# Kernel optimization log

Hardware: AMD Instinct MI355X
Metric: run time of the kernel (lower is better)

The kernel has to match this reference:

```python
import jax, jax.numpy as jnp
import numpy as np

N = 50000      # nodes
E = 800000     # edges (avg degree 16)
IN = 128       # input feature dim
H = 128        # hidden dim (all layers output H; out_channels unused in source)
DROP_P = 0.5


def setup_inputs() -> dict:
    key = jax.random.key(0)
    ks = jax.random.split(key, 8)
    s_in = 1.0 / np.sqrt(IN).astype(np.float32)
    s_h = 1.0 / np.sqrt(H).astype(np.float32)
    return {
        "x": jax.random.normal(ks[0], (N, IN), jnp.float32),
        "edge_index": jax.random.randint(ks[1], (2, E), 0, N, dtype=jnp.int32),
        "Wl0": jax.random.normal(ks[2], (H, IN), jnp.float32) * s_in,
        "bl0": jnp.zeros((H,), jnp.float32),
        "Wr0": jax.random.normal(ks[3], (H, IN), jnp.float32) * s_in,
        "Wl1": jax.random.normal(ks[4], (H, H), jnp.float32) * s_h,
        "bl1": jnp.zeros((H,), jnp.float32),
        "Wr1": jax.random.normal(ks[5], (H, H), jnp.float32) * s_h,
    }


def _sage_conv(x, src, dst, Wl, bl, Wr):
    # mean-aggregate neighbor messages: gather x[src], scatter-add to dst
    agg = jax.ops.segment_sum(x[src], dst, num_segments=N)          # [N, D]
    deg = jax.ops.segment_sum(jnp.ones((src.shape[0],), x.dtype), dst,
                              num_segments=N)                        # [N]
    agg = agg / jnp.maximum(deg, 1.0)[:, None]                       # scatter_mean (0 for isolated nodes)
    # PyG SAGEConv: lin_l(agg) (with bias) + lin_r(x) (no bias)
    return agg @ Wl.T + bl + x @ Wr.T


def reference(x, edge_index, Wl0, bl0, Wr0, Wl1, bl1, Wr1):
    src, dst = edge_index[0], edge_index[1]
    h = _sage_conv(x, src, dst, Wl0, bl0, Wr0)
    h = jax.nn.relu(h)
    # dropout(p=0.5, training=True) with a fixed key for determinism
    keep = jax.random.bernoulli(jax.random.key(42), 1.0 - DROP_P, h.shape)
    h = jnp.where(keep, h / (1.0 - DROP_P), 0.0)
    out = _sage_conv(h, src, dst, Wl1, bl1, Wr1)
    return out
```

## Files before the change

### kernel.cpp

```cpp
#include <hip/hip_runtime.h>
#include <hip/hip_bf16.h>


#define HDIM 128
#define KDIM 256
#define NBUK 256
#define BNODE 196
#define BCAP 4096
#define BCH 2048

typedef __attribute__((ext_vector_type(8))) short bshort8;
typedef __attribute__((ext_vector_type(4))) float f32x4;
typedef __attribute__((ext_vector_type(2))) float f32x2;

__device__ __forceinline__ ushort f2b(float f) {
  __hip_bfloat16 h = __float2bfloat16(f);
  return *(ushort*)&h;
}
__device__ __forceinline__ unsigned int pack2(float lo, float hi) {
  return (unsigned int)f2b(lo) | ((unsigned int)f2b(hi) << 16);
}

#if __has_builtin(__builtin_amdgcn_cvt_pk_f32_fp8) && __has_builtin(__builtin_amdgcn_cvt_pk_fp8_f32)
#define FP8_HW 1
#endif

__device__ __forceinline__ unsigned int fp8e1(float f) {
  unsigned int u = __float_as_uint(f);
  unsigned int s = (u >> 24) & 0x80u;
  unsigned int mag = u & 0x7FFFFFFFu;
  if (mag < 0x38800000u) return s;
  if (mag > 0x43E00000u) mag = 0x43E00000u;
  unsigned int r = mag + 0x7FFFFu + ((mag >> 20) & 1u);
  return s | ((r >> 20) - 960u);
}
__device__ __forceinline__ float fp8d1(unsigned int b) {
  unsigned int v = b & 0x7Fu;
  float fn = __uint_as_float(((b & 0x80u) << 24) | ((v + 960u) << 20));
  return v >= 8u ? fn : 0.0f;
}

__device__ __forceinline__ unsigned int fp8x4_enc(float f0, float f1, float f2, float f3) {
#ifdef FP8_HW
  int u = 0;
  u = __builtin_amdgcn_cvt_pk_fp8_f32(f0, f1, u, false);
  u = __builtin_amdgcn_cvt_pk_fp8_f32(f2, f3, u, true);
  return (unsigned int)u;
#else
  return fp8e1(f0) | (fp8e1(f1) << 8) | (fp8e1(f2) << 16) | (fp8e1(f3) << 24);
#endif
}
__device__ __forceinline__ void fp8x4_acc(float* a, unsigned int w) {
#ifdef FP8_HW
  f32x2 lo = __builtin_amdgcn_cvt_pk_f32_fp8((int)w, false);
  f32x2 hi = __builtin_amdgcn_cvt_pk_f32_fp8((int)w, true);
  a[0] += lo.x; a[1] += lo.y; a[2] += hi.x; a[3] += hi.y;
#else
  a[0] += fp8d1(w & 255u); a[1] += fp8d1((w >> 8) & 255u);
  a[2] += fp8d1((w >> 16) & 255u); a[3] += fp8d1(w >> 24);
#endif
}

__device__ __forceinline__ unsigned int tf_rotl(unsigned int x, int d) {
  return (x << d) | (x >> (32 - d));
}
__device__ __forceinline__ bool dropout_keep(unsigned int j) {
  unsigned int x0 = 0u, x1 = j;
  const unsigned int ks0 = 0u, ks1 = 42u, ks2 = 0x1BD11BDAu ^ 0u ^ 42u;
  x0 += ks0; x1 += ks1;
#define TF_R(r) { x0 += x1; x1 = tf_rotl(x1, (r)); x1 ^= x0; }
  TF_R(13) TF_R(15) TF_R(26) TF_R(6)
  x0 += ks1; x1 += ks2 + 1u;
  TF_R(17) TF_R(29) TF_R(16) TF_R(24)
  x0 += ks2; x1 += ks0 + 2u;
  TF_R(13) TF_R(15) TF_R(26) TF_R(6)
  x0 += ks0; x1 += ks1 + 3u;
  TF_R(17) TF_R(29) TF_R(16) TF_R(24)
  x0 += ks1; x1 += ks2 + 4u;
  TF_R(13) TF_R(15) TF_R(26) TF_R(6)
  x0 += ks2; x1 += ks0 + 5u;
#undef TF_R
  unsigned int r = x0 ^ x1;
  float u = __uint_as_float((r >> 9) | 0x3f800000u) - 1.0f;
  return u < 0.5f;
}

__global__ __launch_bounds__(256) void bin_cvt_k(
    const int* __restrict__ src, const int* __restrict__ dst,
    int* __restrict__ bucketCount, unsigned int* __restrict__ pairs, int E, int EB,
    const float* __restrict__ x,
    const float* __restrict__ Wl0, const float* __restrict__ Wr0,
    const float* __restrict__ Wl1, const float* __restrict__ Wr1,
    ushort* __restrict__ Xb, unsigned char* __restrict__ Xq,
    ushort* __restrict__ Wc0, ushort* __restrict__ Wc1, int N) {
  __shared__ int hist[NBUK];
  __shared__ int lofs[NBUK];
  __shared__ int lcur[NBUK];
  __shared__ int gbase[NBUK];
  __shared__ unsigned int ordv[BCH];
  __shared__ unsigned char ordb[BCH];

  int b = blockIdx.x;
  if (b >= EB) {
    b -= EB;
    if (b < 64) {
      int t = b * 256 + threadIdx.x;
      int o = t >> 7, k = t & 127;
      Wc0[o * KDIM + k] = f2b(Wl0[t]);
      Wc0[o * KDIM + HDIM + k] = f2b(Wr0[t]);
      Wc1[o * KDIM + k] = f2b(Wl1[t]);
      Wc1[o * KDIM + HDIM + k] = f2b(Wr1[t]);
    } else {
      int t = (b - 64) * 256 + threadIdx.x;
      if (t < N * 32) {
        int n = t >> 5, c4 = t & 31;
        float4 v = *(const float4*)&x[(size_t)n * HDIM + c4 * 4];
        uint2 p;
        p.x = pack2(v.x, v.y);
        p.y = pack2(v.z, v.w);
        *(uint2*)&Xb[(size_t)n * HDIM + c4 * 4] = p;
        *(unsigned int*)&Xq[(size_t)n * HDIM + c4 * 4] = fp8x4_enc(v.x, v.y, v.z, v.w);
      }
    }
    return;
  }

  hist[threadIdx.x] = 0;
  __syncthreads();
  int begin = b * BCH;
  int n = min(BCH, E - begin);
  unsigned int vals[BCH / 256];
  int bks[BCH / 256];
  int cnt = 0;
  for (int i = threadIdx.x; i < n; i += 256) {
    int s = src[begin + i], d = dst[begin + i];
    int bk = d / BNODE;
    int dloc = d - bk * BNODE;
    vals[cnt] = ((unsigned int)s << 8) | (unsigned int)dloc;
    bks[cnt] = bk;
    ++cnt;
    atomicAdd(&hist[bk], 1);
  }
  __syncthreads();
  {
    int v = hist[threadIdx.x];
    lofs[threadIdx.x] = v;
    __syncthreads();
    for (int off = 1; off < NBUK; off <<= 1) {
      int t = (threadIdx.x >= off) ? lofs[threadIdx.x - off] : 0;
      __syncthreads();
      lofs[threadIdx.x] += t;
      __syncthreads();
    }
    int ex = lofs[threadIdx.x] - v;
    __syncthreads();
    lofs[threadIdx.x] = ex;
    lcur[threadIdx.x] = ex;
    gbase[threadIdx.x] = atomicAdd(&bucketCount[threadIdx.x], v);
  }
  __syncthreads();
  for (int k = 0; k < cnt; ++k) {
    int bk = bks[k];
    int p = atomicAdd(&lcur[bk], 1);
    ordv[p] = vals[k];
    ordb[p] = (unsigned char)bk;
  }
  __syncthreads();
  for (int j = threadIdx.x; j < n; j += 256) {
    int bk = ordb[j];
    pairs[bk * BCAP + gbase[bk] + (j - lofs[bk])] = ordv[j];
  }
}

__global__ __launch_bounds__(256) void build_k(const unsigned int* __restrict__ pairs,
                                               const int* __restrict__ bucketCount,
                                               int* __restrict__ deg,
                                               int* __restrict__ rowptr,
                                               ushort* __restrict__ eidx, int N) {
  __shared__ int h[BNODE];
  __shared__ int lofs[BNODE];
  __shared__ int cur[BNODE];
  const int b = blockIdx.x;
  const int base = b * BCAP;
  const int cnt = bucketCount[b];
  const int nodebase = b * BNODE;
  const int nloc = min(BNODE, N - nodebase);
  if (threadIdx.x < BNODE) h[threadIdx.x] = 0;
  __syncthreads();
  for (int i = threadIdx.x; i < cnt; i += 256) atomicAdd(&h[pairs[base + i] & 255u], 1);
  __syncthreads();
  if (threadIdx.x < BNODE) lofs[threadIdx.x] = h[threadIdx.x];
  __syncthreads();
  for (int off = 1; off < BNODE; off <<= 1) {
    int t = (threadIdx.x >= off && threadIdx.x < BNODE) ? lofs[threadIdx.x - off] : 0;
    __syncthreads();
    if (threadIdx.x < BNODE) lofs[threadIdx.x] += t;
    __syncthreads();
  }
  if (threadIdx.x < BNODE) {
    int ex = lofs[threadIdx.x] - h[threadIdx.x];
    cur[threadIdx.x] = ex;
    if (threadIdx.x < nloc) {
      deg[nodebase + threadIdx.x] = h[threadIdx.x];
      rowptr[nodebase + threadIdx.x] = base + ex;
    }
  }
  __syncthreads();
  for (int i = threadIdx.x; i < cnt; i += 256) {
    unsigned int v = pairs[base + i];
    int pos = atomicAdd(&cur[v & 255u], 1);
    eidx[base + pos] = (ushort)(v >> 8);
  }
}

__global__ __launch_bounds__(256) void agg_q(const unsigned char* __restrict__ Fq,
                                             ushort* __restrict__ Ag,
                                             const ushort* __restrict__ eidx,
                                             const int* __restrict__ rowptr,
                                             const int* __restrict__ deg, int N) {
  const int lane = threadIdx.x & 63;
  const int n = blockIdx.x * 4 + (threadIdx.x >> 6);
  if (n >= N) return;
  const int start = rowptr[n];
  const int d = deg[n];
  const int es = lane >> 3;
  const int cl = lane & 7;
  float a[16];
#pragma unroll
  for (int i = 0; i < 16; ++i) a[i] = 0.0f;
  for (int j = 0; j < d; j += 16) {
    uint4 v[2];
    bool m[2];
#pragma unroll
    for (int u = 0; u < 2; ++u) {
      int e = j + u * 8 + es;
      m[u] = e < d;
      if (m[u]) {
        int s = eidx[start + e];
        v[u] = *(const uint4*)&Fq[(size_t)s * HDIM + cl * 16];
      }
    }
#pragma unroll
    for (int u = 0; u < 2; ++u)
      if (m[u]) {
        fp8x4_acc(&a[0], v[u].x);
        fp8x4_acc(&a[4], v[u].y);
        fp8x4_acc(&a[8], v[u].z);
        fp8x4_acc(&a[12], v[u].w);
      }
  }
#pragma unroll
  for (int i = 0; i < 16; ++i) {
    a[i] += __shfl_xor(a[i], 8, 64);
    a[i] += __shfl_xor(a[i], 16, 64);
    a[i] += __shfl_xor(a[i], 32, 64);
  }
  if (es == 0) {
    float rd = 1.0f / fmaxf((float)d, 1.0f);
    uint4 p0, p1;
    p0.x = pack2(a[0] * rd, a[1] * rd);
    p0.y = pack2(a[2] * rd, a[3] * rd);
    p0.z = pack2(a[4] * rd, a[5] * rd);
    p0.w = pack2(a[6] * rd, a[7] * rd);
    p1.x = pack2(a[8] * rd, a[9] * rd);
    p1.y = pack2(a[10] * rd, a[11] * rd);
    p1.z = pack2(a[12] * rd, a[13] * rd);
    p1.w = pack2(a[14] * rd, a[15] * rd);
    *(uint4*)&Ag[(size_t)n * HDIM + cl * 16] = p0;
    *(uint4*)&Ag[(size_t)n * HDIM + cl * 16 + 8] = p1;
  }
}

template <int MODE>
__global__ __launch_bounds__(256) void gemm_mfma(const ushort* __restrict__ Agg,
                                                 const ushort* __restrict__ F,
                                                 const ushort* __restrict__ Wc,
                                                 ushort* __restrict__ hb,
                                                 unsigned char* __restrict__ hq,
                                                 float* __restrict__ fout,
                                                 const float* __restrict__ bias,
                                                 int N) {
  __shared__ char smem[34816];
  ushort* Wl = (ushort*)smem;
  float* Tl = (float*)smem;
  const int tid = threadIdx.x;
  const int lane = tid & 63;
  const int wid = tid >> 6;
  const int quad = lane >> 4;
  const int l15 = lane & 15;
  const int n0 = blockIdx.x * 64;

  int rowA = n0 + wid * 16 + l15;
  if (rowA >= N) rowA = N - 1;
  bshort8 afA[4], afF[4];
#pragma unroll
  for (int ks = 0; ks < 4; ++ks) {
    afA[ks] = *(const bshort8*)&Agg[(size_t)rowA * HDIM + ks * 32 + quad * 8];
    afF[ks] = *(const bshort8*)&F[(size_t)rowA * HDIM + ks * 32 + quad * 8];
  }

  f32x4 acc[8];
#pragma unroll
  for (int i = 0; i < 8; ++i) acc[i] = (f32x4){0.f, 0.f, 0.f, 0.f};

#pragma unroll
  for (int half = 0; half < 2; ++half) {
    __syncthreads();
#pragma unroll
    for (int i = 0; i < 8; ++i) {
      int q = i * 256 + tid;
      int row = q >> 4, seg = q & 15;
      *(uint4*)&Wl[row * 136 + seg * 8] = *(const uint4*)&Wc[row * KDIM + half * HDIM + seg * 8];
    }
    __syncthreads();
#pragma unroll
    for (int ks = 0; ks < 4; ++ks) {
#pragma unroll
      for (int os = 0; os < 8; ++os) {
        bshort8 bf = *(const bshort8*)&Wl[(os * 16 + l15) * 136 + ks * 32 + quad * 8];
        acc[os] = __builtin_amdgcn_mfma_f32_16x16x32_bf16(
            half == 0 ? afA[ks] : afF[ks], bf, acc[os], 0, 0, 0);
      }
    }
  }

  __syncthreads();

  const int wbase = wid * (16 * 132);
#pragma unroll
  for (int os = 0; os < 8; ++os)
#pragma unroll
    for (int r = 0; r < 4; ++r)
      Tl[wbase + (quad * 4 + r) * 132 + os * 16 + l15] = acc[os][r];

  __syncthreads();

#pragma unroll
  for (int i = 0; i < 8; ++i) {
    int q = i * 64 + lane;
    int r = q >> 5;
    int c4 = q & 31;
    int n = n0 + wid * 16 + r;
    if (n >= N) continue;
    int c = c4 * 4;
    float4 v = *(float4*)&Tl[wbase + r * 132 + c];
    const float4 bv = *(const float4*)&bias[c];
    v.x += bv.x; v.y += bv.y; v.z += bv.z; v.w += bv.w;
    if (MODE == 1) {
      v.x = v.x > 0.0f ? v.x : 0.0f;
      v.y = v.y > 0.0f ? v.y : 0.0f;
      v.z = v.z > 0.0f ? v.z : 0.0f;
      v.w = v.w > 0.0f ? v.w : 0.0f;
      unsigned int fj = (unsigned int)n * HDIM + (unsigned int)c;
      v.x = dropout_keep(fj + 0u) ? v.x * 2.0f : 0.0f;
      v.y = dropout_keep(fj + 1u) ? v.y * 2.0f : 0.0f;
      v.z = dropout_keep(fj + 2u) ? v.z * 2.0f : 0.0f;
      v.w = dropout_keep(fj + 3u) ? v.w * 2.0f : 0.0f;
      uint2 p;
      p.x = pack2(v.x, v.y);
      p.y = pack2(v.z, v.w);
      *(uint2*)&hb[(size_t)n * HDIM + c] = p;
      *(unsigned int*)&hq[(size_t)n * HDIM + c] = fp8x4_enc(v.x, v.y, v.z, v.w);
    } else {
      *(float4*)&fout[(size_t)n * HDIM + c] = v;
    }
  }
}

extern "C" void kernel_launch(void* const* d_in, const int* in_sizes, int n_in,
                              void* d_out, int out_size, void* d_ws, size_t ws_size,
                              hipStream_t stream) {
  const float* x   = (const float*)d_in[0];
  const int*   ei  = (const int*)d_in[1];
  const float* Wl0 = (const float*)d_in[2];
  const float* bl0 = (const float*)d_in[3];
  const float* Wr0 = (const float*)d_in[4];
  const float* Wl1 = (const float*)d_in[5];
  const float* bl1 = (const float*)d_in[6];
  const float* Wr1 = (const float*)d_in[7];
  float* out = (float*)d_out;

  const int N = in_sizes[0] / HDIM;
  const int E = in_sizes[1] / 2;
  const int* src = ei;
  const int* dst = ei + E;

  const int Na = (N + 63) & ~63;
  int* bucketCount = (int*)d_ws;
  int* deg         = bucketCount + NBUK;
  int* rowptr      = deg + Na;
  unsigned int* pairs = (unsigned int*)(rowptr + Na);
  ushort* eidx     = (ushort*)(pairs + NBUK * BCAP);
  size_t off = (((size_t)(eidx + NBUK * BCAP) - (size_t)d_ws) + 255) & ~(size_t)255;
  ushort* Wc0 = (ushort*)((char*)d_ws + off);
  ushort* Wc1 = Wc0 + 128 * KDIM;
  ushort* Xb  = Wc1 + 128 * KDIM;
  ushort* Hb  = Xb + (size_t)N * HDIM;
  ushort* Ag  = Hb + (size_t)N * HDIM;
  unsigned char* Xq = (unsigned char*)(Ag + (size_t)N * HDIM);
  unsigned char* Hq = Xq + (size_t)N * HDIM;

  hipMemsetAsync(bucketCount, 0, NBUK * sizeof(int), stream);

  const int EB = (E + BCH - 1) / BCH;
  const int GB = (N + 63) / 64;
  const int AB = (N + 3) / 4;
  const int CB = EB + 64 + (N * 32 + 255) / 256;

  bin_cvt_k<<<CB, 256, 0, stream>>>(src, dst, bucketCount, pairs, E, EB,
                                    x, Wl0, Wr0, Wl1, Wr1, Xb, Xq, Wc0, Wc1, N);
  build_k<<<NBUK, 256, 0, stream>>>(pairs, bucketCount, deg, rowptr, eidx, N);

  agg_q<<<AB, 256, 0, stream>>>(Xq, Ag, eidx, rowptr, deg, N);
  gemm_mfma<1><<<GB, 256, 0, stream>>>(Ag, Xb, Wc0, Hb, Hq, nullptr, bl0, N);
  agg_q<<<AB, 256, 0, stream>>>(Hq, Ag, eidx, rowptr, deg, N);
  gemm_mfma<2><<<GB, 256, 0, stream>>>(Ag, Hb, Wc1, nullptr, nullptr, out, bl1, N);
}
```

Measured before the change: 210.6 us.

## Restructure FP8 neighbor aggregation to one edge per wavefront step, two columns per lane

The aggregation kernel now has each wavefront walk the node's edges serially. Each lane owns two feature columns and loads a 2-byte slice of every neighbor row, with four edges in flight and separate accumulators. Before, eight lanes split each row into 16-byte chunks across eight edges, followed by a cross-lane shuffle reduction. The new layout removes the shuffle reduction and the per-edge masking, and stores one 4-byte word per lane. In exchange each gather is many narrow 2-byte loads instead of wide 16-byte loads, and the edge loop is sequential, so memory-level parallelism per wave may drop.

```diff
diff --git a/kernel.cpp b/kernel.cpp
--- a/kernel.cpp
+++ b/kernel.cpp
@@ -50,14 +50,13 @@
   return fp8e1(f0) | (fp8e1(f1) << 8) | (fp8e1(f2) << 16) | (fp8e1(f3) << 24);
 #endif
 }
-__device__ __forceinline__ void fp8x4_acc(float* a, unsigned int w) {
+
+__device__ __forceinline__ void fp8x2_acc(float& a0, float& a1, unsigned int w) {
 #ifdef FP8_HW
   f32x2 lo = __builtin_amdgcn_cvt_pk_f32_fp8((int)w, false);
-  f32x2 hi = __builtin_amdgcn_cvt_pk_f32_fp8((int)w, true);
-  a[0] += lo.x; a[1] += lo.y; a[2] += hi.x; a[3] += hi.y;
+  a0 += lo.x; a1 += lo.y;
 #else
-  a[0] += fp8d1(w & 255u); a[1] += fp8d1((w >> 8) & 255u);
-  a[2] += fp8d1((w >> 16) & 255u); a[3] += fp8d1(w >> 24);
+  a0 += fp8d1(w & 255u); a1 += fp8d1((w >> 8) & 255u);
 #endif
 }
 
@@ -213,7 +212,7 @@
   }
 }
 
-__global__ __launch_bounds__(256) void agg_q(const unsigned char* __restrict__ Fq,
+__global__ __launch_bounds__(256) void agg_c(const unsigned char* __restrict__ Fq,
                                              ushort* __restrict__ Ag,
                                              const ushort* __restrict__ eidx,
                                              const int* __restrict__ rowptr,
@@ -221,54 +220,35 @@
   const int lane = threadIdx.x & 63;
   const int n = blockIdx.x * 4 + (threadIdx.x >> 6);
   if (n >= N) return;
-  const int start = rowptr[n];
-  const int d = deg[n];
-  const int es = lane >> 3;
-  const int cl = lane & 7;
-  float a[16];
-#pragma unroll
-  for (int i = 0; i < 16; ++i) a[i] = 0.0f;
-  for (int j = 0; j < d; j += 16) {
-    uint4 v[2];
-    bool m[2];
-#pragma unroll
-    for (int u = 0; u < 2; ++u) {
-      int e = j + u * 8 + es;
-      m[u] = e < d;
-      if (m[u]) {
-        int s = eidx[start + e];
-        v[u] = *(const uint4*)&Fq[(size_t)s * HDIM + cl * 16];
-      }
-    }
-#pragma unroll
-    for (int u = 0; u < 2; ++u)
-      if (m[u]) {
-        fp8x4_acc(&a[0], v[u].x);
-        fp8x4_acc(&a[4], v[u].y);
-        fp8x4_acc(&a[8], v[u].z);
-        fp8x4_acc(&a[12], v[u].w);
-      }
-  }
-#pragma unroll
-  for (int i = 0; i < 16; ++i) {
-    a[i] += __shfl_xor(a[i], 8, 64);
-    a[i] += __shfl_xor(a[i], 16, 64);
-    a[i] += __shfl_xor(a[i], 32, 64);
-  }
-  if (es == 0) {
-    float rd = 1.0f / fmaxf((float)d, 1.0f);
-    uint4 p0, p1;
-    p0.x = pack2(a[0] * rd, a[1] * rd);
-    p0.y = pack2(a[2] * rd, a[3] * rd);
-    p0.z = pack2(a[4] * rd, a[5] * rd);
-    p0.w = pack2(a[6] * rd, a[7] * rd);
-    p1.x = pack2(a[8] * rd, a[9] * rd);
-    p1.y = pack2(a[10] * rd, a[11] * rd);
-    p1.z = pack2(a[12] * rd, a[13] * rd);
-    p1.w = pack2(a[14] * rd, a[15] * rd);
-    *(uint4*)&Ag[(size_t)n * HDIM + cl * 16] = p0;
-    *(uint4*)&Ag[(size_t)n * HDIM + cl * 16 + 8] = p1;
-  }
+  const int start = __builtin_amdgcn_readfirstlane(rowptr[n]);
+  const int d = __builtin_amdgcn_readfirstlane(deg[n]);
+  const unsigned int co = (unsigned int)(lane << 1);
+  const ushort* ep = eidx + start;
+
+  float a0 = 0.f, a1 = 0.f, b0 = 0.f, b1 = 0.f;
+  float c0 = 0.f, c1 = 0.f, d0 = 0.f, d1 = 0.f;
+  int j = 0;
+  for (; j + 4 <= d; j += 4) {
+    int s0 = ep[j], s1 = ep[j + 1], s2 = ep[j + 2], s3 = ep[j + 3];
+    unsigned int w0 = *(const ushort*)(Fq + (size_t)s0 * HDIM + co);
+    unsigned int w1 = *(const ushort*)(Fq + (size_t)s1 * HDIM + co);
+    unsigned int w2 = *(const ushort*)(Fq + (size_t)s2 * HDIM + co);
+    unsigned int w3 = *(const ushort*)(Fq + (size_t)s3 * HDIM + co);
+    fp8x2_acc(a0, a1, w0);
+    fp8x2_acc(b0, b1, w1);
+    fp8x2_acc(c0, c1, w2);
+    fp8x2_acc(d0, d1, w3);
+  }
+  for (; j < d; ++j) {
+    int s0 = ep[j];
+    unsigned int w0 = *(const ushort*)(Fq + (size_t)s0 * HDIM + co);
+    fp8x2_acc(a0, a1, w0);
+  }
+  a0 += b0; a1 += b1;
+  c0 += d0; c1 += d1;
+  a0 += c0; a1 += c1;
+  const float rd = 1.0f / fmaxf((float)d, 1.0f);
+  *(unsigned int*)&Ag[(size_t)n * HDIM + (lane << 1)] = pack2(a0 * rd, a1 * rd);
 }
 
 template <int MODE>
@@ -411,8 +391,8 @@
                                     x, Wl0, Wr0, Wl1, Wr1, Xb, Xq, Wc0, Wc1, N);
   build_k<<<NBUK, 256, 0, stream>>>(pairs, bucketCount, deg, rowptr, eidx, N);
 
-  agg_q<<<AB, 256, 0, stream>>>(Xq, Ag, eidx, rowptr, deg, N);
+  agg_c<<<AB, 256, 0, stream>>>(Xq, Ag, eidx, rowptr, deg, N);
   gemm_mfma<1><<<GB, 256, 0, stream>>>(Ag, Xb, Wc0, Hb, Hq, nullptr, bl0, N);
-  agg_q<<<AB, 256, 0, stream>>>(Hq, Ag, eidx, rowptr, deg, N);
+  agg_c<<<AB, 256, 0, stream>>>(Hq, Ag, eidx, rowptr, deg, N);
   gemm_mfma<2><<<GB, 256, 0, stream>>>(Ag, Hb, Wc1, nullptr, nullptr, out, bl1, N);
 }
```

Result: slower. 218.1 us (+3.6%).
